# Optimization experiments

Measured on AMD Instinct MI355X. Metric: run time of the kernel, lower is better.

The kernel has to match this reference:

```python
import jax, jax.numpy as jnp
import numpy as np

B, T, D, H = 256, 2048, 64, 64

def setup_inputs() -> dict:
    key = jax.random.key(0)
    ks = jax.random.split(key, 9)
    s_in = 1.0 / np.sqrt(D)
    s_rec = 1.0 / np.sqrt(H)
    return {
        "lstm_input": jax.random.normal(ks[0], (B, T, D), dtype=jnp.float32),
        "inputs_state": jax.random.normal(ks[1], (B, H), dtype=jnp.float32),
        # LSTM kernel/recurrent_kernel/bias, Keras gate order [i, f, c, o]
        "W": jax.random.normal(ks[2], (D, 4 * H), dtype=jnp.float32) * s_in,
        "U": jax.random.normal(ks[3], (H, 4 * H), dtype=jnp.float32) * s_rec,
        "b": jax.random.normal(ks[4], (4 * H,), dtype=jnp.float32) * 0.05,
        # Dense(1) heads
        "w_gamma": jax.random.normal(ks[5], (H, 1), dtype=jnp.float32) * s_rec,
        "b_gamma": jax.random.normal(ks[6], (1,), dtype=jnp.float32) * 0.05,
        "w_beta": jax.random.normal(ks[7], (H, 1), dtype=jnp.float32) * s_rec,
        "b_beta": jax.random.normal(ks[8], (1,), dtype=jnp.float32) * 0.05,
    }

def reference(lstm_input, inputs_state, W, U, b, w_gamma, b_gamma, w_beta, b_beta):
    # Keras LSTM(64, activation='sigmoid'): recurrent_activation=sigmoid (gates),
    # activation=sigmoid (candidate + cell output, replacing the usual tanh).
    # get_initial_state(inputs_state) -> zero h0/c0 (only batch size is used).
    sig = jax.nn.sigmoid
    # Precompute input projections for all timesteps: [B,T,4H]
    xz = jnp.einsum('btd,dg->btg', lstm_input, W) + b

    def step(carry, z_t):
        h, c = carry
        z = z_t + h @ U  # [B,4H]
        i, f, g, o = jnp.split(z, 4, axis=-1)
        c = sig(f) * c + sig(i) * sig(g)
        h = sig(o) * sig(c)
        return (h, c), None

    h0 = jnp.zeros((lstm_input.shape[0], H), dtype=lstm_input.dtype)
    c0 = jnp.zeros_like(h0)
    (h, _), _ = jax.lax.scan(step, (h0, c0), jnp.swapaxes(xz, 0, 1))

    gamma = h @ w_gamma + b_gamma  # [B,1]
    beta = h @ w_beta + b_beta     # [B,1]
    return (gamma, beta)
```

## Files before the change

### kernel.cpp

```cpp
#include <hip/hip_runtime.h>


typedef _Float16 f16;
typedef f16  half8 __attribute__((ext_vector_type(8)));
typedef __fp16 fp16x2 __attribute__((ext_vector_type(2)));
typedef float f32x4 __attribute__((ext_vector_type(4)));

constexpr int Bsz = 256;
constexpr int Tn  = 2048;
constexpr int Dn  = 64;
constexpr int G4  = 256;
constexpr int XZS = 68;

__global__ __launch_bounds__(256, 1) void lstm_film_mfma(
    const float* __restrict__ x,
    const float* __restrict__ W,
    const float* __restrict__ U,
    const float* __restrict__ bias,
    const float* __restrict__ wg, const float* __restrict__ bgam,
    const float* __restrict__ wb, const float* __restrict__ bbet,
    float* __restrict__ out)
{
    __shared__ __align__(16) char hbuf[2][128];
    __shared__ __align__(16) float xzbuf[4][2][16][XZS];

    const int tid  = threadIdx.x;
    const int w    = tid >> 6;
    const int l    = tid & 63;
    const int lrow = l & 15;
    const int kgrp = l >> 4;

    const float NK = -1.44269504f;

    half8 Bf[4][4];
#pragma unroll
    for (int kf = 0; kf < 4; ++kf) {
        const float* M = (kf < 2) ? U : W;
        const int krow0 = (kf & 1) * 32 + kgrp * 8;
#pragma unroll
        for (int q = 0; q < 4; ++q) {
            const int col = q * 64 + w * 16 + lrow;
#pragma unroll
            for (int j = 0; j < 8; ++j)
                Bf[kf][q][j] = (f16)(M[(krow0 + j) * G4 + col] * NK);
        }
    }
    float bq[4];
#pragma unroll
    for (int q = 0; q < 4; ++q) bq[q] = bias[q * 64 + w * 16 + lrow] * NK;

    if (tid < 16) ((uint4*)hbuf)[tid] = uint4{0, 0, 0, 0};
    float c = 0.0f;

    const float* xlane = x + ((size_t)blockIdx.x * Tn + lrow) * Dn + kgrp * 8;

    const int rdH0 = kgrp * 16;
    const int rdH1 = kgrp * 16 + 64;
    const int wrH  = (w * 16 + lrow) * 2;

    float* xzw = &xzbuf[w][0][0][0];

    const float wgj = wg[l], wbj = wb[l];
    const float bg0 = bgam[0], bb0 = bbet[0];

    __syncthreads();

#define XL(R, T0) do {                                                       \
        const float* p_ = xlane + (size_t)(T0) * Dn;                         \
        R[0] = *(const float4*)(p_);      R[1] = *(const float4*)(p_ + 4);   \
        R[2] = *(const float4*)(p_ + 32); R[3] = *(const float4*)(p_ + 36);  \
    } while (0)

#define XBLOCK(R, X) do {                                                    \
        union { fp16x2 p[4]; half8 h8; } u0, u1;                             \
        u0.p[0] = __builtin_amdgcn_cvt_pkrtz(R[0].x, R[0].y);                \
        u0.p[1] = __builtin_amdgcn_cvt_pkrtz(R[0].z, R[0].w);                \
        u0.p[2] = __builtin_amdgcn_cvt_pkrtz(R[1].x, R[1].y);                \
        u0.p[3] = __builtin_amdgcn_cvt_pkrtz(R[1].z, R[1].w);                \
        u1.p[0] = __builtin_amdgcn_cvt_pkrtz(R[2].x, R[2].y);                \
        u1.p[1] = __builtin_amdgcn_cvt_pkrtz(R[2].z, R[2].w);                \
        u1.p[2] = __builtin_amdgcn_cvt_pkrtz(R[3].x, R[3].y);                \
        u1.p[3] = __builtin_amdgcn_cvt_pkrtz(R[3].z, R[3].w);                \
        f32x4 q0 = {bq[0], bq[0], bq[0], bq[0]};                             \
        f32x4 q1 = {bq[1], bq[1], bq[1], bq[1]};                             \
        f32x4 q2 = {bq[2], bq[2], bq[2], bq[2]};                             \
        f32x4 q3 = {bq[3], bq[3], bq[3], bq[3]};                             \
        q0 = __builtin_amdgcn_mfma_f32_16x16x32_f16(u0.h8, Bf[2][0], q0,0,0,0);\
        q1 = __builtin_amdgcn_mfma_f32_16x16x32_f16(u0.h8, Bf[2][1], q1,0,0,0);\
        q2 = __builtin_amdgcn_mfma_f32_16x16x32_f16(u0.h8, Bf[2][2], q2,0,0,0);\
        q3 = __builtin_amdgcn_mfma_f32_16x16x32_f16(u0.h8, Bf[2][3], q3,0,0,0);\
        q0 = __builtin_amdgcn_mfma_f32_16x16x32_f16(u1.h8, Bf[3][0], q0,0,0,0);\
        q1 = __builtin_amdgcn_mfma_f32_16x16x32_f16(u1.h8, Bf[3][1], q1,0,0,0);\
        q2 = __builtin_amdgcn_mfma_f32_16x16x32_f16(u1.h8, Bf[3][2], q2,0,0,0);\
        q3 = __builtin_amdgcn_mfma_f32_16x16x32_f16(u1.h8, Bf[3][3], q3,0,0,0);\
        float* bp = xzw + (X) * (16 * XZS);                                  \
        _Pragma("unroll")                                                    \
        for (int r = 0; r < 4; ++r) {                                        \
            f32x4 tv; tv[0] = q0[r]; tv[1] = q1[r];                          \
            tv[2] = q2[r]; tv[3] = q3[r];                                    \
            *(f32x4*)(bp + (4 * kgrp + r) * XZS + lrow * 4) = tv;            \
        }                                                                    \
    } while (0)

#define HSTEP(S, X) do {                                                     \
        asm volatile("s_waitcnt lgkmcnt(0)" ::: "memory");                   \
        __builtin_amdgcn_s_barrier();                                        \
        asm volatile("" ::: "memory");                                       \
        const char* hb = hbuf[(S) & 1];                                      \
        half8 ah0 = *(const half8*)(hb + rdH0);                              \
        half8 ah1 = *(const half8*)(hb + rdH1);                              \
        f32x4 v = *(const f32x4*)(xzw + (X) * (16 * XZS) + (S) * XZS + lrow * 4);\
        f32x4 a0 = v;                                                        \
        f32x4 a1 = v; a1[0] = v[1];                                          \
        f32x4 a2 = v; a2[0] = v[2];                                          \
        f32x4 a3 = v; a3[0] = v[3];                                          \
        a0 = __builtin_amdgcn_mfma_f32_16x16x32_f16(ah0, Bf[0][0], a0,0,0,0);\
        a1 = __builtin_amdgcn_mfma_f32_16x16x32_f16(ah0, Bf[0][1], a1,0,0,0);\
        a2 = __builtin_amdgcn_mfma_f32_16x16x32_f16(ah0, Bf[0][2], a2,0,0,0);\
        a3 = __builtin_amdgcn_mfma_f32_16x16x32_f16(ah0, Bf[0][3], a3,0,0,0);\
        a0 = __builtin_amdgcn_mfma_f32_16x16x32_f16(ah1, Bf[1][0], a0,0,0,0);\
        a1 = __builtin_amdgcn_mfma_f32_16x16x32_f16(ah1, Bf[1][1], a1,0,0,0);\
        a2 = __builtin_amdgcn_mfma_f32_16x16x32_f16(ah1, Bf[1][2], a2,0,0,0);\
        a3 = __builtin_amdgcn_mfma_f32_16x16x32_f16(ah1, Bf[1][3], a3,0,0,0);\
        const float ei = __builtin_amdgcn_exp2f(a0[0]);                      \
        const float ef = __builtin_amdgcn_exp2f(a1[0]);                      \
        const float eg = __builtin_amdgcn_exp2f(a2[0]);                      \
        const float eo = __builtin_amdgcn_exp2f(a3[0]);                      \
        const float sf  = __builtin_amdgcn_rcpf(1.0f + ef);                  \
        const float sig = __builtin_amdgcn_rcpf((1.0f + ei) * (1.0f + eg));  \
        c = fmaf(sf, c, sig);                                                \
        const float ec = __builtin_amdgcn_exp2f(c * NK);                     \
        const float hh = __builtin_amdgcn_rcpf((1.0f + eo) * (1.0f + ec));   \
        *(f16*)(hbuf[((S) & 1) ^ 1] + wrH) = (f16)hh;                        \
    } while (0)

    float4 R[4];
    XL(R, 0);
    XBLOCK(R, 0);
    XL(R, 16);

    for (int tb = 0; tb < Tn / 16; ++tb) {
        const int X = tb & 1;
#pragma unroll
        for (int s = 0; s < 16; ++s) {
            if (s == 14 && tb < Tn / 16 - 1) {
                XBLOCK(R, X ^ 1);
                const int tn = (tb + 2) * 16;
                XL(R, tn < Tn ? tn : Tn - 16);
            }
            HSTEP(s, X);
        }
    }
#undef HSTEP
#undef XBLOCK
#undef XL

    __syncthreads();

    if (w == 0) {
        const float hv = (float)*(const f16*)(hbuf[0] + l * 2);
        float vg = hv * wgj, vb = hv * wbj;
#pragma unroll
        for (int off = 32; off > 0; off >>= 1) {
            vg += __shfl_xor(vg, off, 64);
            vb += __shfl_xor(vb, off, 64);
        }
        if (l == 0) {
            out[blockIdx.x]       = vg + bg0;
            out[Bsz + blockIdx.x] = vb + bb0;
        }
    }
}

extern "C" void kernel_launch(void* const* d_in, const int* in_sizes, int n_in,
                              void* d_out, int out_size, void* d_ws, size_t ws_size,
                              hipStream_t stream) {
    const float* x    = (const float*)d_in[0];
    const float* W    = (const float*)d_in[2];
    const float* U    = (const float*)d_in[3];
    const float* bias = (const float*)d_in[4];
    const float* wg   = (const float*)d_in[5];
    const float* bgam = (const float*)d_in[6];
    const float* wb   = (const float*)d_in[7];
    const float* bbet = (const float*)d_in[8];
    float* out = (float*)d_out;

    lstm_film_mfma<<<Bsz, 256, 0, stream>>>(x, W, U, bias,
                                            wg, bgam, wb, bbet, out);
}
```

Before: 502.8 us.

## Keep input projections in registers and interleave their MFMAs across recurrent steps

Removes the LDS staging buffer for precomputed x·W projections. The input-projection MFMAs for the next 16-step block are now spread one per recurrent step into the dependency-bound loop, and their results are held in double-buffered registers (qA/qB). Each lane takes its own accumulator row (S&3) per step. Because lane ownership of h changes every 4 steps, the cell state c is handed off through a small LDS array. Only the owning kgrp writes h. This trades LDS stores and loads plus the bulk XBLOCK stall for extra per-step indexing and an LDS round-trip for c every 4 steps.

```diff
diff --git a/kernel.cpp b/kernel.cpp
--- a/kernel.cpp
+++ b/kernel.cpp
@@ -10,7 +10,6 @@
 constexpr int Tn  = 2048;
 constexpr int Dn  = 64;
 constexpr int G4  = 256;
-constexpr int XZS = 68;
 
 __global__ __launch_bounds__(256, 1) void lstm_film_mfma(
     const float* __restrict__ x,
@@ -22,7 +21,7 @@
     float* __restrict__ out)
 {
     __shared__ __align__(16) char hbuf[2][128];
-    __shared__ __align__(16) float xzbuf[4][2][16][XZS];
+    __shared__ __align__(16) float c_lds[64];
 
     const int tid  = threadIdx.x;
     const int w    = tid >> 6;
@@ -45,114 +44,124 @@
                 Bf[kf][q][j] = (f16)(M[(krow0 + j) * G4 + col] * NK);
         }
     }
-    float bq[4];
+    f32x4 bqv[4];
 #pragma unroll
-    for (int q = 0; q < 4; ++q) bq[q] = bias[q * 64 + w * 16 + lrow] * NK;
+    for (int q = 0; q < 4; ++q) {
+        const float b = bias[q * 64 + w * 16 + lrow] * NK;
+        bqv[q] = f32x4{b, b, b, b};
+    }
+    const f32x4 ZV = {0.f, 0.f, 0.f, 0.f};
 
     if (tid < 16) ((uint4*)hbuf)[tid] = uint4{0, 0, 0, 0};
+    if (tid < 64) c_lds[tid] = 0.0f;
     float c = 0.0f;
 
     const float* xlane = x + ((size_t)blockIdx.x * Tn + lrow) * Dn + kgrp * 8;
-
     const int rdH0 = kgrp * 16;
     const int rdH1 = kgrp * 16 + 64;
     const int wrH  = (w * 16 + lrow) * 2;
-
-    float* xzw = &xzbuf[w][0][0][0];
+    const int cidx = w * 16 + lrow;
 
     const float wgj = wg[l], wbj = wb[l];
     const float bg0 = bgam[0], bb0 = bbet[0];
 
     __syncthreads();
 
-#define XL(R, T0) do {                                                       \
-        const float* p_ = xlane + (size_t)(T0) * Dn;                         \
+    union U16 { fp16x2 p[4]; half8 h8; };
+    U16 u0, u1;
+    float4 R[4];
+    f32x4 qA0, qA1, qA2, qA3, qB0, qB1, qB2, qB3;
+
+#define XL(T0) do { const float* p_ = xlane + (size_t)(T0) * Dn;             \
         R[0] = *(const float4*)(p_);      R[1] = *(const float4*)(p_ + 4);   \
         R[2] = *(const float4*)(p_ + 32); R[3] = *(const float4*)(p_ + 36);  \
     } while (0)
 
-#define XBLOCK(R, X) do {                                                    \
-        union { fp16x2 p[4]; half8 h8; } u0, u1;                             \
+#define CVT0 do {                                                            \
         u0.p[0] = __builtin_amdgcn_cvt_pkrtz(R[0].x, R[0].y);                \
         u0.p[1] = __builtin_amdgcn_cvt_pkrtz(R[0].z, R[0].w);                \
         u0.p[2] = __builtin_amdgcn_cvt_pkrtz(R[1].x, R[1].y);                \
-        u0.p[3] = __builtin_amdgcn_cvt_pkrtz(R[1].z, R[1].w);                \
+        u0.p[3] = __builtin_amdgcn_cvt_pkrtz(R[1].z, R[1].w); } while (0)
+#define CVT1 do {                                                            \
         u1.p[0] = __builtin_amdgcn_cvt_pkrtz(R[2].x, R[2].y);                \
         u1.p[1] = __builtin_amdgcn_cvt_pkrtz(R[2].z, R[2].w);                \
         u1.p[2] = __builtin_amdgcn_cvt_pkrtz(R[3].x, R[3].y);                \
-        u1.p[3] = __builtin_amdgcn_cvt_pkrtz(R[3].z, R[3].w);                \
-        f32x4 q0 = {bq[0], bq[0], bq[0], bq[0]};                             \
-        f32x4 q1 = {bq[1], bq[1], bq[1], bq[1]};                             \
-        f32x4 q2 = {bq[2], bq[2], bq[2], bq[2]};                             \
-        f32x4 q3 = {bq[3], bq[3], bq[3], bq[3]};                             \
-        q0 = __builtin_amdgcn_mfma_f32_16x16x32_f16(u0.h8, Bf[2][0], q0,0,0,0);\
-        q1 = __builtin_amdgcn_mfma_f32_16x16x32_f16(u0.h8, Bf[2][1], q1,0,0,0);\
-        q2 = __builtin_amdgcn_mfma_f32_16x16x32_f16(u0.h8, Bf[2][2], q2,0,0,0);\
-        q3 = __builtin_amdgcn_mfma_f32_16x16x32_f16(u0.h8, Bf[2][3], q3,0,0,0);\
-        q0 = __builtin_amdgcn_mfma_f32_16x16x32_f16(u1.h8, Bf[3][0], q0,0,0,0);\
-        q1 = __builtin_amdgcn_mfma_f32_16x16x32_f16(u1.h8, Bf[3][1], q1,0,0,0);\
-        q2 = __builtin_amdgcn_mfma_f32_16x16x32_f16(u1.h8, Bf[3][2], q2,0,0,0);\
-        q3 = __builtin_amdgcn_mfma_f32_16x16x32_f16(u1.h8, Bf[3][3], q3,0,0,0);\
-        float* bp = xzw + (X) * (16 * XZS);                                  \
-        _Pragma("unroll")                                                    \
-        for (int r = 0; r < 4; ++r) {                                        \
-            f32x4 tv; tv[0] = q0[r]; tv[1] = q1[r];                          \
-            tv[2] = q2[r]; tv[3] = q3[r];                                    \
-            *(f32x4*)(bp + (4 * kgrp + r) * XZS + lrow * 4) = tv;            \
-        }                                                                    \
-    } while (0)
+        u1.p[3] = __builtin_amdgcn_cvt_pkrtz(R[3].z, R[3].w); } while (0)
 
-#define HSTEP(S, X) do {                                                     \
+#define MFM __builtin_amdgcn_mfma_f32_16x16x32_f16
+
+#define HSTEP(S, Q, ...) do {                                                \
         asm volatile("s_waitcnt lgkmcnt(0)" ::: "memory");                   \
         __builtin_amdgcn_s_barrier();                                        \
         asm volatile("" ::: "memory");                                       \
-        const char* hb = hbuf[(S) & 1];                                      \
-        half8 ah0 = *(const half8*)(hb + rdH0);                              \
-        half8 ah1 = *(const half8*)(hb + rdH1);                              \
-        f32x4 v = *(const f32x4*)(xzw + (X) * (16 * XZS) + (S) * XZS + lrow * 4);\
-        f32x4 a0 = v;                                                        \
-        f32x4 a1 = v; a1[0] = v[1];                                          \
-        f32x4 a2 = v; a2[0] = v[2];                                          \
-        f32x4 a3 = v; a3[0] = v[3];                                          \
-        a0 = __builtin_amdgcn_mfma_f32_16x16x32_f16(ah0, Bf[0][0], a0,0,0,0);\
-        a1 = __builtin_amdgcn_mfma_f32_16x16x32_f16(ah0, Bf[0][1], a1,0,0,0);\
-        a2 = __builtin_amdgcn_mfma_f32_16x16x32_f16(ah0, Bf[0][2], a2,0,0,0);\
-        a3 = __builtin_amdgcn_mfma_f32_16x16x32_f16(ah0, Bf[0][3], a3,0,0,0);\
-        a0 = __builtin_amdgcn_mfma_f32_16x16x32_f16(ah1, Bf[1][0], a0,0,0,0);\
-        a1 = __builtin_amdgcn_mfma_f32_16x16x32_f16(ah1, Bf[1][1], a1,0,0,0);\
-        a2 = __builtin_amdgcn_mfma_f32_16x16x32_f16(ah1, Bf[1][2], a2,0,0,0);\
-        a3 = __builtin_amdgcn_mfma_f32_16x16x32_f16(ah1, Bf[1][3], a3,0,0,0);\
-        const float ei = __builtin_amdgcn_exp2f(a0[0]);                      \
-        const float ef = __builtin_amdgcn_exp2f(a1[0]);                      \
-        const float eg = __builtin_amdgcn_exp2f(a2[0]);                      \
-        const float eo = __builtin_amdgcn_exp2f(a3[0]);                      \
+        const char* hb_ = hbuf[(S) & 1];                                     \
+        half8 ah0 = *(const half8*)(hb_ + rdH0);                             \
+        half8 ah1 = *(const half8*)(hb_ + rdH1);                             \
+        if (((S) & 3) == 0) c = c_lds[cidx];                                 \
+        f32x4 a0 = MFM(ah0, Bf[0][0], bqv[0], 0, 0, 0);                      \
+        f32x4 a1 = MFM(ah0, Bf[0][1], bqv[1], 0, 0, 0);                      \
+        f32x4 a2 = MFM(ah0, Bf[0][2], bqv[2], 0, 0, 0);                      \
+        f32x4 a3 = MFM(ah0, Bf[0][3], bqv[3], 0, 0, 0);                      \
+        a0 = MFM(ah1, Bf[1][0], a0, 0, 0, 0);                                \
+        a1 = MFM(ah1, Bf[1][1], a1, 0, 0, 0);                                \
+        a2 = MFM(ah1, Bf[1][2], a2, 0, 0, 0);                                \
+        a3 = MFM(ah1, Bf[1][3], a3, 0, 0, 0);                                \
+        __VA_ARGS__                                                          \
+        const float zi = Q##0[(S) & 3] + a0[(S) & 3];                        \
+        const float zf = Q##1[(S) & 3] + a1[(S) & 3];                        \
+        const float zg = Q##2[(S) & 3] + a2[(S) & 3];                        \
+        const float zo = Q##3[(S) & 3] + a3[(S) & 3];                        \
+        const float ei = __builtin_amdgcn_exp2f(zi);                         \
+        const float ef = __builtin_amdgcn_exp2f(zf);                         \
+        const float eg = __builtin_amdgcn_exp2f(zg);                         \
+        const float eo = __builtin_amdgcn_exp2f(zo);                         \
         const float sf  = __builtin_amdgcn_rcpf(1.0f + ef);                  \
         const float sig = __builtin_amdgcn_rcpf((1.0f + ei) * (1.0f + eg));  \
         c = fmaf(sf, c, sig);                                                \
         const float ec = __builtin_amdgcn_exp2f(c * NK);                     \
         const float hh = __builtin_amdgcn_rcpf((1.0f + eo) * (1.0f + ec));   \
-        *(f16*)(hbuf[((S) & 1) ^ 1] + wrH) = (f16)hh;                        \
+        if (kgrp == ((S) >> 2)) {                                            \
+            *(f16*)(hbuf[((S) & 1) ^ 1] + wrH) = (f16)hh;                    \
+            if (((S) & 3) == 3) c_lds[cidx] = c;                             \
+        }                                                                    \
     } while (0)
 
-    float4 R[4];
-    XL(R, 0);
-    XBLOCK(R, 0);
-    XL(R, 16);
+#define BLOCK16(QC, QN, TNX)                                                 \
+        HSTEP(0, QC);  HSTEP(1, QC);  HSTEP(2, QC);  HSTEP(3, QC);           \
+        HSTEP(4, QC);  HSTEP(5, QC);  HSTEP(6, QC);  HSTEP(7, QC);           \
+        HSTEP(8, QC,  CVT0; QN##0 = MFM(u0.h8, Bf[2][0], ZV, 0, 0, 0); );    \
+        HSTEP(9, QC,        QN##1 = MFM(u0.h8, Bf[2][1], ZV, 0, 0, 0); );    \
+        HSTEP(10, QC,       QN##2 = MFM(u0.h8, Bf[2][2], ZV, 0, 0, 0); );    \
+        HSTEP(11, QC,       QN##3 = MFM(u0.h8, Bf[2][3], ZV, 0, 0, 0); );    \
+        HSTEP(12, QC, CVT1; QN##0 = MFM(u1.h8, Bf[3][0], QN##0, 0, 0, 0); ); \
+        HSTEP(13, QC,       QN##1 = MFM(u1.h8, Bf[3][1], QN##1, 0, 0, 0);    \
+                            XL(TNX); );                                      \
+        HSTEP(14, QC,       QN##2 = MFM(u1.h8, Bf[3][2], QN##2, 0, 0, 0); ); \
+        HSTEP(15, QC,       QN##3 = MFM(u1.h8, Bf[3][3], QN##3, 0, 0, 0); );
 
-    for (int tb = 0; tb < Tn / 16; ++tb) {
-        const int X = tb & 1;
-#pragma unroll
-        for (int s = 0; s < 16; ++s) {
-            if (s == 14 && tb < Tn / 16 - 1) {
-                XBLOCK(R, X ^ 1);
-                const int tn = (tb + 2) * 16;
-                XL(R, tn < Tn ? tn : Tn - 16);
-            }
-            HSTEP(s, X);
-        }
+    XL(0);
+    CVT0; CVT1;
+    qA0 = MFM(u0.h8, Bf[2][0], ZV, 0, 0, 0);
+    qA1 = MFM(u0.h8, Bf[2][1], ZV, 0, 0, 0);
+    qA2 = MFM(u0.h8, Bf[2][2], ZV, 0, 0, 0);
+    qA3 = MFM(u0.h8, Bf[2][3], ZV, 0, 0, 0);
+    qA0 = MFM(u1.h8, Bf[3][0], qA0, 0, 0, 0);
+    qA1 = MFM(u1.h8, Bf[3][1], qA1, 0, 0, 0);
+    qA2 = MFM(u1.h8, Bf[3][2], qA2, 0, 0, 0);
+    qA3 = MFM(u1.h8, Bf[3][3], qA3, 0, 0, 0);
+    XL(16);
+
+    for (int tb = 0; tb < Tn / 16; tb += 2) {
+        int t2 = (tb + 2) * 16; if (t2 > Tn - 16) t2 = Tn - 16;
+        int t3 = (tb + 3) * 16; if (t3 > Tn - 16) t3 = Tn - 16;
+        BLOCK16(qA, qB, t2)
+        BLOCK16(qB, qA, t3)
     }
+#undef BLOCK16
 #undef HSTEP
-#undef XBLOCK
+#undef MFM
+#undef CVT0
+#undef CVT1
 #undef XL
 
     __syncthreads();
```

Result: faster. 456.0 us (-9.3%).
